# Performance work log

Hardware: AMD Instinct MI355X
Metric: run time of the kernel (lower is better)

The kernel has to match this reference:

```python
import jax, jax.numpy as jnp
import numpy as np

B, T, IN, H, L = 256, 512, 64, 128, 2

def _lstm_layer(x_tbi, w_ih, w_hh, b_ih, b_hh):
    # x_tbi: [T, B, in]; weights follow PyTorch layout: w_ih [4H, in], w_hh [4H, H]
    # Precompute input projections for all timesteps (one big GEMM).
    xg = jnp.einsum('tbi,gi->tbg', x_tbi, w_ih) + b_ih + b_hh  # [T, B, 4H]
    h0 = jnp.zeros((x_tbi.shape[1], w_hh.shape[1]), x_tbi.dtype)
    c0 = jnp.zeros_like(h0)
    def step(carry, xg_t):
        h, c = carry
        gates = xg_t + h @ w_hh.T  # [B, 4H]
        i, f, g, o = jnp.split(gates, 4, axis=-1)  # PyTorch gate order i,f,g,o
        i, f, o = jax.nn.sigmoid(i), jax.nn.sigmoid(f), jax.nn.sigmoid(o)
        c = f * c + i * jnp.tanh(g)
        h = o * jnp.tanh(c)
        return (h, c), h
    (_, _), hs = jax.lax.scan(step, (h0, c0), xg)
    return hs  # [T, B, H]

def setup_inputs() -> dict:
    key = jax.random.key(0)
    ks = jax.random.split(key, 12)
    s = 1.0 / np.sqrt(H)
    u = lambda k, shape: jax.random.uniform(k, shape, jnp.float32, -s, s)
    return {
        'x': jax.random.normal(ks[0], (B, T, IN), jnp.float32),
        'w_ih0': u(ks[1], (4 * H, IN)), 'w_hh0': u(ks[2], (4 * H, H)),
        'b_ih0': u(ks[3], (4 * H,)),   'b_hh0': u(ks[4], (4 * H,)),
        'w_ih1': u(ks[5], (4 * H, H)), 'w_hh1': u(ks[6], (4 * H, H)),
        'b_ih1': u(ks[7], (4 * H,)),   'b_hh1': u(ks[8], (4 * H,)),
        'fc_w': u(ks[9], (1, H)),      'fc_b': u(ks[10], (1,)),
    }

def reference(x, w_ih0, w_hh0, b_ih0, b_hh0, w_ih1, w_hh1, b_ih1, b_hh1, fc_w, fc_b):
    h = jnp.transpose(x, (1, 0, 2))  # [T, B, IN]
    h = _lstm_layer(h, w_ih0, w_hh0, b_ih0, b_hh0)
    h = _lstm_layer(h, w_ih1, w_hh1, b_ih1, b_hh1)
    last = h[-1]  # [B, H] == x[:, -1, :] in batch_first layout
    return last @ fc_w.T + fc_b  # [B, 1]
```

## Files before the change

kernel.cpp:

```cpp
#include <hip/hip_runtime.h>
#include <hip/hip_fp16.h>


#define TT 512
#define CH 8
#define NCH 64
#define MM (256 * 512)
#define HP 136

typedef _Float16 f16x4 __attribute__((ext_vector_type(4)));
typedef _Float16 f16x8 __attribute__((ext_vector_type(8)));
typedef float f32x4 __attribute__((ext_vector_type(4)));

__device__ __forceinline__ float tanh_f(float x) {
    float e = __expf(2.0f * x);
    return 1.0f - 2.0f * __builtin_amdgcn_rcpf(e + 1.0f);
}
__device__ __forceinline__ float sigm_f(float x) {
    return __builtin_amdgcn_rcpf(1.0f + __expf(-x));
}
__device__ __forceinline__ f16x8 cvt8(float4 a, float4 b) {
    f16x8 f;
    f[0] = (_Float16)a.x; f[1] = (_Float16)a.y;
    f[2] = (_Float16)a.z; f[3] = (_Float16)a.w;
    f[4] = (_Float16)b.x; f[5] = (_Float16)b.y;
    f[6] = (_Float16)b.z; f[7] = (_Float16)b.w;
    return f;
}

__global__ void cvt_f32_f16(const float* __restrict__ src,
                            _Float16* __restrict__ dst, int n4) {
    int i = blockIdx.x * blockDim.x + threadIdx.x;
    int stride = gridDim.x * blockDim.x;
    for (; i < n4; i += stride) {
        float4 v = ((const float4*)src)[i];
        f16x4 a;
        a[0] = (_Float16)v.x; a[1] = (_Float16)v.y;
        a[2] = (_Float16)v.z; a[3] = (_Float16)v.w;
        ((f16x4*)dst)[i] = a;
    }
}

__global__ __launch_bounds__(256, 1) void gemm_xg0(
    const float* __restrict__ A32, const _Float16* __restrict__ W,
    const float* __restrict__ bih, const float* __restrict__ bhh,
    _Float16* __restrict__ out)
{
    const int l  = threadIdx.x & 63;
    const int w  = threadIdx.x >> 6;
    const int mb = blockIdx.x * 64 + w * 16;
    const int c  = l & 15;
    const int q  = l >> 4;

    __shared__ float biasl[512];
    for (int i = threadIdx.x; i < 512; i += 256) biasl[i] = bih[i] + bhh[i];
    __syncthreads();

    f32x4 C[32];
    #pragma unroll
    for (int i = 0; i < 32; ++i) C[i] = (f32x4){0.f, 0.f, 0.f, 0.f};

    #pragma unroll
    for (int ks = 0; ks < 2; ++ks) {
        const float* ap = A32 + (size_t)(mb + c) * 64 + ks * 32 + q * 8;
        f16x8 Af = cvt8(((const float4*)ap)[0], ((const float4*)ap)[1]);
        #pragma unroll
        for (int nt = 0; nt < 32; ++nt) {
            f16x8 Bf = *(const f16x8*)(W + (size_t)(nt * 16 + c) * 64 + ks * 32 + q * 8);
            C[nt] = __builtin_amdgcn_mfma_f32_16x16x32_f16(Af, Bf, C[nt], 0, 0, 0);
        }
    }
    #pragma unroll
    for (int uu = 0; uu < 8; ++uu) {
        float b0 = biasl[uu * 16 + c];
        float b1 = biasl[128 + uu * 16 + c];
        float b2 = biasl[256 + uu * 16 + c];
        float b3 = biasl[384 + uu * 16 + c];
        #pragma unroll
        for (int i = 0; i < 4; ++i) {
            int row = mb + q * 4 + i;
            f16x4 pk;
            pk[0] = (_Float16)(C[uu][i]      + b0);
            pk[1] = (_Float16)(C[8 + uu][i]  + b1);
            pk[2] = (_Float16)(C[16 + uu][i] + b2);
            pk[3] = (_Float16)(C[24 + uu][i] + b3);
            ((f16x4*)out)[(size_t)row * 128 + uu * 16 + c] = pk;
        }
    }
}

__global__
__attribute__((amdgpu_flat_work_group_size(512, 512), amdgpu_waves_per_eu(2, 2)))
void lstm_fused(
    const float* __restrict__ whh0, const float* __restrict__ wih1,
    const float* __restrict__ whh1,
    const float* __restrict__ bih1, const float* __restrict__ bhh1,
    const _Float16* __restrict__ xg0,
    const float* __restrict__ fc_w, const float* __restrict__ fc_b,
    float* __restrict__ out)
{
    const int t = threadIdx.x;
    const int b = blockIdx.x;
    const int w = t >> 6;
    const int l = t & 63;
    const int q = l >> 4;
    const int c = l & 15;
    const int unit = (w << 4) + c;

    __shared__ __align__(16) _Float16 w1lds[512 * 128];
    __shared__ __align__(16) _Float16 xg1t[CH * 512];
    __shared__ __align__(16) _Float16 h0tile[CH * HP];
    __shared__ __align__(16) _Float16 h1buf[2][128];
    __shared__ float redbuf[128];

    {
        const int r = t;
        const float* src = wih1 + (size_t)r * 128;
        #pragma unroll
        for (int j = 0; j < 16; ++j)
            *(f16x8*)&w1lds[r * 128 + ((j ^ (r & 7)) << 3)] =
                cvt8(((const float4*)src)[2 * j], ((const float4*)src)[2 * j + 1]);
    }

    f16x8 B0[4][4], B1[4][4];
    #pragma unroll
    for (int g = 0; g < 4; ++g) {
        #pragma unroll
        for (int kt = 0; kt < 4; ++kt) {
            const size_t off = (size_t)((g << 7) + unit) * 128 + (kt << 5) + (q << 3);
            B0[g][kt] = cvt8(((const float4*)(whh0 + off))[0],
                             ((const float4*)(whh0 + off))[1]);
            B1[g][kt] = cvt8(((const float4*)(whh1 + off))[0],
                             ((const float4*)(whh1 + off))[1]);
        }
    }
    float bias1g[4];
    #pragma unroll
    for (int g = 0; g < 4; ++g)
        bias1g[g] = bih1[(g << 7) + unit] + bhh1[(g << 7) + unit];

    {
        int i = t;
        ((float4*)xg1t)[i] = make_float4(0.f, 0.f, 0.f, 0.f);
    }
    if (t < 128) {
        h1buf[0][t] = (_Float16)0.f;
        h1buf[1][t] = (_Float16)0.f;
        h0tile[(CH - 1) * HP + t] = (_Float16)0.f;
    }

    const f16x4* __restrict__ xgp = (const f16x4*)xg0 + (size_t)b * TT * 128 + unit;
    f16x4 xr[4];
    xr[0] = xgp[0];
    xr[1] = xgp[128];
    xr[2] = xr[0]; xr[3] = xr[0];

    f32x4 a0[4], a1[4];
    #pragma unroll
    for (int g = 0; g < 4; ++g) {
        a0[g] = (f32x4){0.f, 0.f, 0.f, 0.f};
        a1[g] = (f32x4){0.f, 0.f, 0.f, 0.f};
    }
    float cst0 = 0.f, cst1 = 0.f;
    __syncthreads();

    #pragma unroll 1
    for (int k = 0; k <= NCH; ++k) {
        #pragma unroll
        for (int j = 0; j < CH; ++j) {
            const int rp = (j + CH - 1) & (CH - 1);
            f16x4 xv  = xr[j & 3];
            f16x4 x1v = *(const f16x4*)&xg1t[(j << 9) + (unit << 2)];
            #pragma unroll
            for (int g = 0; g < 4; ++g) {
                a0[g][0] = (float)xv[g];
                a1[g][0] = (float)x1v[g];
            }
            xr[(j + 2) & 3] = xgp[(size_t)(k * CH + j + 2) * 128];

            #pragma unroll
            for (int kt = 0; kt < 4; ++kt) {
                f16x8 Af0 = *(const f16x8*)&h0tile[rp * HP + (kt << 5) + (q << 3)];
                f16x8 Af1 = *(const f16x8*)&h1buf[(j & 1) ^ 1][(kt << 5) + (q << 3)];
                #pragma unroll
                for (int g = 0; g < 4; ++g)
                    a0[g] = __builtin_amdgcn_mfma_f32_16x16x32_f16(Af0, B0[g][kt], a0[g], 0, 0, 0);
                #pragma unroll
                for (int g = 0; g < 4; ++g)
                    a1[g] = __builtin_amdgcn_mfma_f32_16x16x32_f16(Af1, B1[g][kt], a1[g], 0, 0, 0);
            }
            {
                float gi = sigm_f(a0[0][0]);
                float gf = sigm_f(a0[1][0]);
                float gg = tanh_f(a0[2][0]);
                float go = sigm_f(a0[3][0]);
                cst0 = gf * cst0 + gi * gg;
                float hh = go * tanh_f(cst0);
                if (l < 16) h0tile[j * HP + unit] = (_Float16)hh;
            }
            {
                float gi = sigm_f(a1[0][0]);
                float gf = sigm_f(a1[1][0]);
                float gg = tanh_f(a1[2][0]);
                float go = sigm_f(a1[3][0]);
                cst1 = gf * cst1 + gi * gg;
                float hh = go * tanh_f(cst1);
                if (l < 16) {
                    h1buf[j & 1][unit] = (_Float16)hh;
                    if (j == CH - 1) redbuf[unit] = hh;
                }
            }
            __syncthreads();
        }

        if (k < NCH) {
            f32x4 G[4];
            #pragma unroll
            for (int g = 0; g < 4; ++g)
                G[g] = (f32x4){bias1g[g], bias1g[g], bias1g[g], bias1g[g]};
            #pragma unroll
            for (int kt = 0; kt < 4; ++kt) {
                f16x8 Ah = *(const f16x8*)&h0tile[(c & 7) * HP + (kt << 5) + (q << 3)];
                #pragma unroll
                for (int g = 0; g < 4; ++g) {
                    f16x8 Bg = *(const f16x8*)&w1lds[(((g << 7) + unit) << 7) +
                                   ((((kt << 2) + q) ^ (c & 7)) << 3)];
                    G[g] = __builtin_amdgcn_mfma_f32_16x16x32_f16(Ah, Bg, G[g], 0, 0, 0);
                }
            }
            #pragma unroll
            for (int i2 = 0; i2 < 4; ++i2) {
                f16x4 pk;
                pk[0] = (_Float16)G[0][i2]; pk[1] = (_Float16)G[1][i2];
                pk[2] = (_Float16)G[2][i2]; pk[3] = (_Float16)G[3][i2];
                *(f16x4*)&xg1t[((((q << 2) + i2) & 7) << 9) + (unit << 2)] = pk;
            }
            __syncthreads();
        }
    }

    if (t < 64) {
        float p = redbuf[t] * fc_w[t] + redbuf[t + 64] * fc_w[t + 64];
        #pragma unroll
        for (int off = 32; off > 0; off >>= 1) p += __shfl_down(p, off, 64);
        if (t == 0) out[b] = p + fc_b[0];
    }
}

extern "C" void kernel_launch(void* const* d_in, const int* in_sizes, int n_in,
                              void* d_out, int out_size, void* d_ws, size_t ws_size,
                              hipStream_t stream) {
    const float* x     = (const float*)d_in[0];
    const float* w_ih0 = (const float*)d_in[1];
    const float* w_hh0 = (const float*)d_in[2];
    const float* b_ih0 = (const float*)d_in[3];
    const float* b_hh0 = (const float*)d_in[4];
    const float* w_ih1 = (const float*)d_in[5];
    const float* w_hh1 = (const float*)d_in[6];
    const float* b_ih1 = (const float*)d_in[7];
    const float* b_hh1 = (const float*)d_in[8];
    const float* fc_w  = (const float*)d_in[9];
    const float* fc_b  = (const float*)d_in[10];
    float* out = (float*)d_out;

    char* ws = (char*)d_ws;
    _Float16* xg    = (_Float16*)(ws);
    _Float16* w0_16 = (_Float16*)(ws + 134217728 + 65536);

    cvt_f32_f16<<<dim3(32), dim3(256), 0, stream>>>(w_ih0, w0_16, (512 * 64) / 4);

    gemm_xg0<<<dim3(MM / 64), dim3(256), 0, stream>>>(x, w0_16, b_ih0, b_hh0, xg);

    lstm_fused<<<dim3(256), dim3(512), 0, stream>>>(w_hh0, w_ih1, w_hh1,
                                                    b_ih1, b_hh1, xg,
                                                    fc_w, fc_b, out);
}
```

Measured before the change: 643.2 us.

## Split LSTM layers across separate wave groups in 1024-thread block

Doubles the block to 1024 threads so waves 0-7 run the layer-0 recurrence and the layer-1 input projection, while waves 8-15 run the layer-1 recurrence. Each wave then holds only one set of recurrent weights in registers instead of two. The layer-0 waves skip their step in the drain chunk. Plain __syncthreads is replaced by an explicit lgkmcnt wait plus s_barrier. The intent is to raise per-step parallelism and cut register pressure, at the cost of a larger block barrier across 16 waves and idle layer-1 waves during the projection phase.

```diff
diff --git a/kernel.cpp b/kernel.cpp
--- a/kernel.cpp
+++ b/kernel.cpp
@@ -11,6 +11,11 @@
 typedef _Float16 f16x4 __attribute__((ext_vector_type(4)));
 typedef _Float16 f16x8 __attribute__((ext_vector_type(8)));
 typedef float f32x4 __attribute__((ext_vector_type(4)));
+
+__device__ __forceinline__ void bar_lgkm() {
+    asm volatile("s_waitcnt lgkmcnt(0)" ::: "memory");
+    __builtin_amdgcn_s_barrier();
+}
 
 __device__ __forceinline__ float tanh_f(float x) {
     float e = __expf(2.0f * x);
@@ -89,9 +94,7 @@
     }
 }
 
-__global__
-__attribute__((amdgpu_flat_work_group_size(512, 512), amdgpu_waves_per_eu(2, 2)))
-void lstm_fused(
+__global__ __launch_bounds__(1024) void lstm_fused(
     const float* __restrict__ whh0, const float* __restrict__ wih1,
     const float* __restrict__ whh1,
     const float* __restrict__ bih1, const float* __restrict__ bhh1,
@@ -101,11 +104,12 @@
 {
     const int t = threadIdx.x;
     const int b = blockIdx.x;
-    const int w = t >> 6;
+    const int wid = t >> 6;
     const int l = t & 63;
     const int q = l >> 4;
     const int c = l & 15;
-    const int unit = (w << 4) + c;
+    const bool isL1 = wid >= 8;
+    const int unit = ((wid & 7) << 4) + c;
 
     __shared__ __align__(16) _Float16 w1lds[512 * 128];
     __shared__ __align__(16) _Float16 xg1t[CH * 512];
@@ -114,35 +118,36 @@
     __shared__ float redbuf[128];
 
     {
-        const int r = t;
-        const float* src = wih1 + (size_t)r * 128;
-        #pragma unroll
-        for (int j = 0; j < 16; ++j)
+        const int r = t >> 1;
+        const int jb = (t & 1) << 3;
+        const float4* src = (const float4*)(wih1 + (size_t)r * 128);
+        #pragma unroll
+        for (int j2 = 0; j2 < 8; ++j2) {
+            const int j = jb + j2;
             *(f16x8*)&w1lds[r * 128 + ((j ^ (r & 7)) << 3)] =
-                cvt8(((const float4*)src)[2 * j], ((const float4*)src)[2 * j + 1]);
-    }
-
-    f16x8 B0[4][4], B1[4][4];
+                cvt8(src[2 * j], src[2 * j + 1]);
+        }
+    }
+
+    const float* whh = isL1 ? whh1 : whh0;
+    f16x8 B[4][4];
     #pragma unroll
     for (int g = 0; g < 4; ++g) {
         #pragma unroll
         for (int kt = 0; kt < 4; ++kt) {
             const size_t off = (size_t)((g << 7) + unit) * 128 + (kt << 5) + (q << 3);
-            B0[g][kt] = cvt8(((const float4*)(whh0 + off))[0],
-                             ((const float4*)(whh0 + off))[1]);
-            B1[g][kt] = cvt8(((const float4*)(whh1 + off))[0],
-                             ((const float4*)(whh1 + off))[1]);
+            B[g][kt] = cvt8(((const float4*)(whh + off))[0],
+                            ((const float4*)(whh + off))[1]);
         }
     }
     float bias1g[4];
-    #pragma unroll
-    for (int g = 0; g < 4; ++g)
-        bias1g[g] = bih1[(g << 7) + unit] + bhh1[(g << 7) + unit];
-
-    {
-        int i = t;
-        ((float4*)xg1t)[i] = make_float4(0.f, 0.f, 0.f, 0.f);
-    }
+    if (!isL1) {
+        #pragma unroll
+        for (int g = 0; g < 4; ++g)
+            bias1g[g] = bih1[(g << 7) + unit] + bhh1[(g << 7) + unit];
+    }
+
+    if (t < 512) ((float4*)xg1t)[t] = make_float4(0.f, 0.f, 0.f, 0.f);
     if (t < 128) {
         h1buf[0][t] = (_Float16)0.f;
         h1buf[1][t] = (_Float16)0.f;
@@ -151,17 +156,16 @@
 
     const f16x4* __restrict__ xgp = (const f16x4*)xg0 + (size_t)b * TT * 128 + unit;
     f16x4 xr[4];
-    xr[0] = xgp[0];
-    xr[1] = xgp[128];
-    xr[2] = xr[0]; xr[3] = xr[0];
-
-    f32x4 a0[4], a1[4];
-    #pragma unroll
-    for (int g = 0; g < 4; ++g) {
-        a0[g] = (f32x4){0.f, 0.f, 0.f, 0.f};
-        a1[g] = (f32x4){0.f, 0.f, 0.f, 0.f};
-    }
-    float cst0 = 0.f, cst1 = 0.f;
+    if (!isL1) {
+        xr[0] = xgp[0];
+        xr[1] = xgp[128];
+        xr[2] = xr[0]; xr[3] = xr[0];
+    }
+
+    f32x4 a[4];
+    #pragma unroll
+    for (int g = 0; g < 4; ++g) a[g] = (f32x4){0.f, 0.f, 0.f, 0.f};
+    float cst = 0.f;
     __syncthreads();
 
     #pragma unroll 1
@@ -169,73 +173,65 @@
         #pragma unroll
         for (int j = 0; j < CH; ++j) {
             const int rp = (j + CH - 1) & (CH - 1);
-            f16x4 xv  = xr[j & 3];
-            f16x4 x1v = *(const f16x4*)&xg1t[(j << 9) + (unit << 2)];
-            #pragma unroll
-            for (int g = 0; g < 4; ++g) {
-                a0[g][0] = (float)xv[g];
-                a1[g][0] = (float)x1v[g];
+            if (isL1 || (k < NCH)) {
+                f16x4 xv;
+                if (isL1) xv = *(const f16x4*)&xg1t[(j << 9) + (unit << 2)];
+                else      xv = xr[j & 3];
+                #pragma unroll
+                for (int g = 0; g < 4; ++g) a[g][0] = (float)xv[g];
+                if (!isL1)
+                    xr[(j + 2) & 3] = xgp[(size_t)(k * CH + j + 2) * 128];
+
+                const _Float16* hp = isL1 ? &h1buf[(j & 1) ^ 1][0]
+                                          : &h0tile[rp * HP];
+                #pragma unroll
+                for (int kt = 0; kt < 4; ++kt) {
+                    f16x8 Af = *(const f16x8*)&hp[(kt << 5) + (q << 3)];
+                    #pragma unroll
+                    for (int g = 0; g < 4; ++g)
+                        a[g] = __builtin_amdgcn_mfma_f32_16x16x32_f16(Af, B[g][kt], a[g], 0, 0, 0);
+                }
+                float gi = sigm_f(a[0][0]);
+                float gf = sigm_f(a[1][0]);
+                float gg = tanh_f(a[2][0]);
+                float go = sigm_f(a[3][0]);
+                cst = gf * cst + gi * gg;
+                float hh = go * tanh_f(cst);
+                if (l < 16) {
+                    _Float16* wp = isL1 ? &h1buf[j & 1][unit]
+                                        : &h0tile[j * HP + unit];
+                    *wp = (_Float16)hh;
+                    if (isL1 && k == NCH && j == CH - 1) redbuf[unit] = hh;
+                }
             }
-            xr[(j + 2) & 3] = xgp[(size_t)(k * CH + j + 2) * 128];
-
-            #pragma unroll
-            for (int kt = 0; kt < 4; ++kt) {
-                f16x8 Af0 = *(const f16x8*)&h0tile[rp * HP + (kt << 5) + (q << 3)];
-                f16x8 Af1 = *(const f16x8*)&h1buf[(j & 1) ^ 1][(kt << 5) + (q << 3)];
+            bar_lgkm();
+        }
+
+        if (k < NCH) {
+            if (!isL1) {
+                f32x4 G[4];
                 #pragma unroll
                 for (int g = 0; g < 4; ++g)
-                    a0[g] = __builtin_amdgcn_mfma_f32_16x16x32_f16(Af0, B0[g][kt], a0[g], 0, 0, 0);
-                #pragma unroll
-                for (int g = 0; g < 4; ++g)
-                    a1[g] = __builtin_amdgcn_mfma_f32_16x16x32_f16(Af1, B1[g][kt], a1[g], 0, 0, 0);
+                    G[g] = (f32x4){bias1g[g], bias1g[g], bias1g[g], bias1g[g]};
+                #pragma unroll
+                for (int kt = 0; kt < 4; ++kt) {
+                    f16x8 Ah = *(const f16x8*)&h0tile[(c & 7) * HP + (kt << 5) + (q << 3)];
+                    #pragma unroll
+                    for (int g = 0; g < 4; ++g) {
+                        f16x8 Bg = *(const f16x8*)&w1lds[(((g << 7) + unit) << 7) +
+                                       ((((kt << 2) + q) ^ (c & 7)) << 3)];
+                        G[g] = __builtin_amdgcn_mfma_f32_16x16x32_f16(Ah, Bg, G[g], 0, 0, 0);
+                    }
+                }
+                #pragma unroll
+                for (int i2 = 0; i2 < 4; ++i2) {
+                    f16x4 pk;
+                    pk[0] = (_Float16)G[0][i2]; pk[1] = (_Float16)G[1][i2];
+                    pk[2] = (_Float16)G[2][i2]; pk[3] = (_Float16)G[3][i2];
+                    *(f16x4*)&xg1t[((((q << 2) + i2) & 7) << 9) + (unit << 2)] = pk;
+                }
             }
-            {
-                float gi = sigm_f(a0[0][0]);
-                float gf = sigm_f(a0[1][0]);
-                float gg = tanh_f(a0[2][0]);
-                float go = sigm_f(a0[3][0]);
-                cst0 = gf * cst0 + gi * gg;
-                float hh = go * tanh_f(cst0);
-                if (l < 16) h0tile[j * HP + unit] = (_Float16)hh;
-            }
-            {
-                float gi = sigm_f(a1[0][0]);
-                float gf = sigm_f(a1[1][0]);
-                float gg = tanh_f(a1[2][0]);
-                float go = sigm_f(a1[3][0]);
-                cst1 = gf * cst1 + gi * gg;
-                float hh = go * tanh_f(cst1);
-                if (l < 16) {
-                    h1buf[j & 1][unit] = (_Float16)hh;
-                    if (j == CH - 1) redbuf[unit] = hh;
-                }
-            }
-            __syncthreads();
-        }
-
-        if (k < NCH) {
-            f32x4 G[4];
-            #pragma unroll
-            for (int g = 0; g < 4; ++g)
-                G[g] = (f32x4){bias1g[g], bias1g[g], bias1g[g], bias1g[g]};
-            #pragma unroll
-            for (int kt = 0; kt < 4; ++kt) {
-                f16x8 Ah = *(const f16x8*)&h0tile[(c & 7) * HP + (kt << 5) + (q << 3)];
-                #pragma unroll
-                for (int g = 0; g < 4; ++g) {
-                    f16x8 Bg = *(const f16x8*)&w1lds[(((g << 7) + unit) << 7) +
-                                   ((((kt << 2) + q) ^ (c & 7)) << 3)];
-                    G[g] = __builtin_amdgcn_mfma_f32_16x16x32_f16(Ah, Bg, G[g], 0, 0, 0);
-                }
-            }
-            #pragma unroll
-            for (int i2 = 0; i2 < 4; ++i2) {
-                f16x4 pk;
-                pk[0] = (_Float16)G[0][i2]; pk[1] = (_Float16)G[1][i2];
-                pk[2] = (_Float16)G[2][i2]; pk[3] = (_Float16)G[3][i2];
-                *(f16x4*)&xg1t[((((q << 2) + i2) & 7) << 9) + (unit << 2)] = pk;
-            }
-            __syncthreads();
+            bar_lgkm();
         }
     }
 
@@ -271,7 +267,7 @@
 
     gemm_xg0<<<dim3(MM / 64), dim3(256), 0, stream>>>(x, w0_16, b_ih0, b_hh0, xg);
 
-    lstm_fused<<<dim3(256), dim3(512), 0, stream>>>(w_hh0, w_ih1, w_hh1,
-                                                    b_ih1, b_hh1, xg,
-                                                    fc_w, fc_b, out);
-}
+    lstm_fused<<<dim3(256), dim3(1024), 0, stream>>>(w_hh0, w_ih1, w_hh1,
+                                                     b_ih1, b_hh1, xg,
+                                                     fc_w, fc_b, out);
+}
```

After: 728.4 us. 13.2% more time.
